# Kernel tuning notes

Measured on AMD Instinct MI355X. Metric: run time of the kernel, lower is better.

The kernel has to match this reference:

```python
import jax, jax.numpy as jnp
import numpy as np
from jax import lax

D_MODEL = 1024
N_GROUPS = 8
SUB_SIZE = 8192
TOP_K = 32
BATCH = 2048


def setup_inputs() -> dict:
    key = jax.random.key(0)
    kx, ke, kb, kd = jax.random.split(key, 4)
    x = jax.random.normal(kx, (BATCH, D_MODEL), dtype=jnp.float32)
    # encoder weights: torch Linear(d_model, size) -> W_enc[g]: [d_model, size]
    W_enc = jax.random.normal(ke, (N_GROUPS, D_MODEL, SUB_SIZE), dtype=jnp.float32) * (1.0 / np.sqrt(D_MODEL))
    b_enc = jax.random.normal(kb, (N_GROUPS, SUB_SIZE), dtype=jnp.float32) * 0.01
    # decoder weights: torch Linear(size, d_model, bias=False).weight is [d_model, size];
    # init normalizes over dim=0 (d_model). We store W_dec[g]: [size, d_model] (= weight.T),
    # so normalize over the last axis.
    W_dec = jax.random.normal(kd, (N_GROUPS, SUB_SIZE, D_MODEL), dtype=jnp.float32)
    W_dec = W_dec / (jnp.linalg.norm(W_dec, axis=-1, keepdims=True) + 1e-8)
    return {"x": x, "W_enc": W_enc, "b_enc": b_enc, "W_dec": W_dec}


def reference(x, W_enc, b_enc, W_dec):
    G, B, S = N_GROUPS, x.shape[0], SUB_SIZE
    # per-group encode: [G, B, S]
    pre = jnp.einsum('bd,gds->gbs', x, W_enc) + b_enc[:, None, :]
    # top-k mask per group (same k for all groups -> batched lax.top_k)
    _, idxs = lax.top_k(pre, TOP_K)  # idxs: [G, B, k]
    gi = jnp.arange(G)[:, None, None]
    bi = jnp.arange(B)[None, :, None]
    mask = jnp.zeros_like(pre).at[gi, bi, idxs].set(1.0)
    acts = jax.nn.relu(pre) * mask  # [G, B, S]
    # per-group decode, summed across groups: [B, d_model]
    final_recon = jnp.einsum('gbs,gsd->bd', acts, W_dec)
    # concatenation of per-group acts along feature dim: [B, G*S]
    full_acts = jnp.transpose(acts, (1, 0, 2)).reshape(B, G * S)
    return (final_recon, full_acts)
```

## Files before the change

kernel.cpp:

```cpp
#include <hip/hip_runtime.h>

#define D_MODEL 1024
#define NGROUPS 8
#define SUB 8192
#define TOPK 32
#define BATCH 2048
#define NTOT (NGROUPS * SUB)

typedef float v4f __attribute__((ext_vector_type(4)));
typedef _Float16 f16x8 __attribute__((ext_vector_type(8)));
typedef _Float16 f16x4 __attribute__((ext_vector_type(4)));
typedef float f32x4 __attribute__((ext_vector_type(4)));

__device__ __forceinline__ unsigned fkey(float f) {
    unsigned u = __float_as_uint(f);
    return (u & 0x80000000u) ? ~u : (u | 0x80000000u);
}
__device__ __forceinline__ float inv_fkey(unsigned key) {
    unsigned u = (key & 0x80000000u) ? (key & 0x7FFFFFFFu) : ~key;
    return __uint_as_float(u);
}

__global__ __launch_bounds__(256) void cvt_x_h(
    const float* __restrict__ x, _Float16* __restrict__ xh)
{
    const size_t i = ((size_t)blockIdx.x * 256 + threadIdx.x) * 8;
    const v4f a = *(const v4f*)(x + i);
    const v4f b = *(const v4f*)(x + i + 4);
    f16x8 h;
#pragma unroll
    for (int j = 0; j < 4; ++j) { h[j] = (_Float16)a[j]; h[4 + j] = (_Float16)b[j]; }
    *(f16x8*)(xh + i) = h;
}

__global__ __launch_bounds__(256) void cvt_wdec_h(
    const float* __restrict__ Wd, _Float16* __restrict__ Wh)
{
    const size_t i = ((size_t)blockIdx.x * 256 + threadIdx.x) * 8;
    const v4f a = *(const v4f*)(Wd + i);
    const v4f b = *(const v4f*)(Wd + i + 4);
    f16x8 h;
#pragma unroll
    for (int j = 0; j < 4; ++j) { h[j] = (_Float16)a[j]; h[4 + j] = (_Float16)b[j]; }
    *(f16x8*)(Wh + i) = h;
}

__global__ __launch_bounds__(256) void transpose_wenc2(
    const float* __restrict__ W, float* __restrict__ WT, _Float16* __restrict__ WhT)
{
    __shared__ float t[32][33];
    const int g = blockIdx.z, kt = blockIdx.y, st = blockIdx.x;
    const int lx = threadIdx.x & 31, ly = threadIdx.x >> 5;
    const float* Wg = W + (size_t)g * D_MODEL * SUB;
    float* WTg = WT + (size_t)g * SUB * D_MODEL;
    _Float16* WhTg = WhT + (size_t)g * SUB * D_MODEL;
#pragma unroll
    for (int r = 0; r < 4; ++r)
        t[ly + 8 * r][lx] = Wg[(size_t)(kt * 32 + ly + 8 * r) * SUB + st * 32 + lx];
    __syncthreads();
#pragma unroll
    for (int r = 0; r < 4; ++r) {
        const float v = t[lx][ly + 8 * r];
        const size_t o = (size_t)(st * 32 + ly + 8 * r) * D_MODEL + kt * 32 + lx;
        WTg[o] = v;
        WhTg[o] = (_Float16)v;
    }
}

__global__ __launch_bounds__(256) void mfma_scores_h2(
    const _Float16* __restrict__ xh, const _Float16* __restrict__ WhT,
    const float* __restrict__ b_enc, float* __restrict__ out_acts)
{
    __shared__ _Float16 Ah[128 * 40];
    __shared__ _Float16 Bh[128 * 40];

    const int tid = threadIdx.x;
    const int wblk = blockIdx.x;
    const int t = (wblk & 7) * 1024 + (wblk >> 3);
    const int mt = t & 15, nt = t >> 4;
    const int g = nt >> 6;
    const int sbase = (nt & 63) * 128;
    const int mbase = mt * 128;

    const int lane = tid & 63, w = tid >> 6;
    const int wm = w >> 1, wn = w & 1;
    const int l15 = lane & 15, grp = lane >> 4;

    const int sr = tid >> 1, kh16 = (tid & 1) * 16;

    const _Float16* Agp = xh + (size_t)mbase * D_MODEL;
    const _Float16* Bgp = WhT + ((size_t)g * SUB + sbase) * D_MODEL;

    f32x4 acc[4][4];
#pragma unroll
    for (int i = 0; i < 4; ++i)
#pragma unroll
        for (int j = 0; j < 4; ++j) acc[i][j] = (f32x4){0.f, 0.f, 0.f, 0.f};

#pragma unroll 1
    for (int it = 0; it < 32; ++it) {
        const int k0 = it * 32;
        const f16x8 a0 = *(const f16x8*)(Agp + (size_t)sr * D_MODEL + k0 + kh16);
        const f16x8 a1 = *(const f16x8*)(Agp + (size_t)sr * D_MODEL + k0 + kh16 + 8);
        const f16x8 b0 = *(const f16x8*)(Bgp + (size_t)sr * D_MODEL + k0 + kh16);
        const f16x8 b1 = *(const f16x8*)(Bgp + (size_t)sr * D_MODEL + k0 + kh16 + 8);

        *(f16x8*)&Ah[sr * 40 + kh16]     = a0;
        *(f16x8*)&Ah[sr * 40 + kh16 + 8] = a1;
        *(f16x8*)&Bh[sr * 40 + kh16]     = b0;
        *(f16x8*)&Bh[sr * 40 + kh16 + 8] = b1;
        __syncthreads();

        f16x8 af[4], bf[4];
#pragma unroll
        for (int i = 0; i < 4; ++i)
            af[i] = *(const f16x8*)&Ah[(wm * 64 + i * 16 + l15) * 40 + 8 * grp];
#pragma unroll
        for (int j = 0; j < 4; ++j)
            bf[j] = *(const f16x8*)&Bh[(wn * 64 + j * 16 + l15) * 40 + 8 * grp];
#pragma unroll
        for (int i = 0; i < 4; ++i)
#pragma unroll
            for (int j = 0; j < 4; ++j)
                acc[i][j] = __builtin_amdgcn_mfma_f32_16x16x32_f16(af[i], bf[j], acc[i][j], 0, 0, 0);
        __syncthreads();
    }

    float bb[4];
#pragma unroll
    for (int j = 0; j < 4; ++j)
        bb[j] = b_enc[(size_t)g * SUB + sbase + wn * 64 + j * 16 + l15];
#pragma unroll
    for (int i = 0; i < 4; ++i) {
        const int row = mbase + wm * 64 + i * 16 + grp * 4;
#pragma unroll
        for (int j = 0; j < 4; ++j) {
            const int cols = sbase + wn * 64 + j * 16 + l15;
#pragma unroll
            for (int r = 0; r < 4; ++r) {
                _Float16* hg = (_Float16*)(out_acts + (size_t)(row + r) * NTOT + (size_t)g * SUB);
                hg[cols] = (_Float16)__fadd_rn(acc[i][j][r], bb[j]);
            }
        }
    }
}

#define CCAP 128
#define BCAP 512

__global__ __launch_bounds__(256) void select_decode_h4(
    const float* __restrict__ x, const float* __restrict__ WT,
    const float* __restrict__ b_enc, const _Float16* __restrict__ Wd_h,
    float* __restrict__ out_recon, float* __restrict__ out_acts)
{
    __shared__ float xrow[1024];
    __shared__ unsigned hist[256], sscan[256], wsum[4];
    __shared__ unsigned sh_bin, sh_above, cert_cnt, band_cnt;
    __shared__ int   cert_idx[CCAP];
    __shared__ float cert_val[CCAP];
    __shared__ int   band_idx[BCAP];
    __shared__ float band_val[BCAP];
    __shared__ int   gcend[4], gbend[4];
    __shared__ int   sel_idx[TOPK];
    __shared__ float sel_val[TOPK];

    const int tid = threadIdx.x;
    const int lane = tid & 63;
    const int w = tid >> 6;
    const size_t b = blockIdx.x >> 1;
    const int h = blockIdx.x & 1;
    const int g0 = h * 4;

    *(float4*)&xrow[tid * 4] = *(const float4*)(x + b * D_MODEL + tid * 4);
    if (tid == 0) { cert_cnt = 0; band_cnt = 0; }
    float r0 = 0.f, r1 = 0.f, r2 = 0.f, r3 = 0.f;

    for (int gi = 0; gi < 4; ++gi) {
        const int g = g0 + gi;
        const _Float16* hg = (const _Float16*)(out_acts + b * NTOT + (size_t)g * SUB);
        float sc[32];
#pragma unroll
        for (int t = 0; t < 4; ++t) {
            const f16x8 hv = *(const f16x8*)(hg + (size_t)(tid + t * 256) * 8);
#pragma unroll
            for (int e = 0; e < 8; ++e) sc[t * 8 + e] = (float)hv[e];
        }

        hist[tid] = 0;
        __syncthreads();
#pragma unroll
        for (int j = 0; j < 32; ++j)
            atomicAdd(&hist[fkey(sc[j]) >> 24], 1u);
        __syncthreads();

        unsigned prefix = 0, kwant = TOPK;
#pragma unroll
        for (int r = 0; r < 2; ++r) {
            unsigned s = hist[tid];
#pragma unroll
            for (int off = 1; off < 64; off <<= 1) {
                const unsigned o = __shfl_down(s, off, 64);
                if (lane + off < 64) s += o;
            }
            if (lane == 0) wsum[w] = s;
            __syncthreads();
            unsigned add = 0;
            for (int w2 = w + 1; w2 < 4; ++w2) add += wsum[w2];
            s += add;
            sscan[tid] = s;
            __syncthreads();
            const unsigned snext = (tid < 255) ? sscan[tid + 1] : 0u;
            if (s >= kwant && snext < kwant) { sh_bin = (unsigned)tid; sh_above = snext; }
            __syncthreads();
            const int shift = 24 - 8 * r;
            prefix |= sh_bin << shift;
            kwant -= sh_above;
            __syncthreads();
            if (r == 0) {
                hist[tid] = 0;
                __syncthreads();
#pragma unroll
                for (int j = 0; j < 32; ++j) {
                    const unsigned key = fkey(sc[j]);
                    if ((key >> 24) == (prefix >> 24))
                        atomicAdd(&hist[(key >> 16) & 255u], 1u);
                }
                __syncthreads();
            }
        }
        const float F = inv_fkey(prefix);
        const unsigned supkey = fkey(F - 0.06f);
        const unsigned inkey  = fkey(F + 0.077f);

#pragma unroll
        for (int j = 0; j < 32; ++j) {
            const unsigned key = fkey(sc[j]);
            if (key >= supkey) {
                const int sidx = (tid + (j >> 3) * 256) * 8 + (j & 7);
                if (key > inkey) {
                    const unsigned slot = atomicAdd(&cert_cnt, 1u);
                    if (slot < CCAP) { cert_idx[slot] = (g << 13) | sidx; cert_val[slot] = fmaxf(sc[j], 0.f); }
                } else {
                    const unsigned slot = atomicAdd(&band_cnt, 1u);
                    if (slot < BCAP) band_idx[slot] = (g << 13) | sidx;
                }
            }
        }
        __syncthreads();
        if (tid == 0) { gcend[gi] = (int)min(cert_cnt, (unsigned)CCAP);
                        gbend[gi] = (int)min(band_cnt, (unsigned)BCAP); }
        __syncthreads();
    }

    float* rowb = out_acts + b * NTOT + (size_t)g0 * SUB;
#pragma unroll 8
    for (int t = 0; t < 32; ++t)
        *(float4*)(rowb + (size_t)(tid + t * 256) * 4) = make_float4(0.f, 0.f, 0.f, 0.f);
    __syncthreads();

    const int bcnt = gbend[3];
    for (int base = 0; base < bcnt; base += 256) {
        const int c = base + tid;
        if (c < bcnt) {
            const int id = band_idx[c];
            const int g = id >> 13, sidx = id & 8191;
            const float* col = WT + ((size_t)g * SUB + sidx) * D_MODEL;
            float a0 = 0.f, a1 = 0.f, a2 = 0.f;
#pragma unroll 4
            for (int q = 0; q < 64; ++q) {
                const float4 w0 = *(const float4*)(col + q * 4);
                const float4 w1 = *(const float4*)(col + 384 + q * 4);
                const float4 w2 = *(const float4*)(col + 768 + q * 4);
                a0 = fmaf(xrow[q * 4 + 0], w0.x, a0); a1 = fmaf(xrow[384 + q * 4 + 0], w1.x, a1); a2 = fmaf(xrow[768 + q * 4 + 0], w2.x, a2);
                a0 = fmaf(xrow[q * 4 + 1], w0.y, a0); a1 = fmaf(xrow[384 + q * 4 + 1], w1.y, a1); a2 = fmaf(xrow[768 + q * 4 + 1], w2.y, a2);
                a0 = fmaf(xrow[q * 4 + 2], w0.z, a0); a1 = fmaf(xrow[384 + q * 4 + 2], w1.z, a1); a2 = fmaf(xrow[768 + q * 4 + 2], w2.z, a2);
                a0 = fmaf(xrow[q * 4 + 3], w0.w, a0); a1 = fmaf(xrow[384 + q * 4 + 3], w1.w, a1); a2 = fmaf(xrow[768 + q * 4 + 3], w2.w, a2);
            }
#pragma unroll 4
            for (int q = 64; q < 96; ++q) {
                const float4 w0 = *(const float4*)(col + q * 4);
                const float4 w1 = *(const float4*)(col + 384 + q * 4);
                a0 = fmaf(xrow[q * 4 + 0], w0.x, a0); a1 = fmaf(xrow[384 + q * 4 + 0], w1.x, a1);
                a0 = fmaf(xrow[q * 4 + 1], w0.y, a0); a1 = fmaf(xrow[384 + q * 4 + 1], w1.y, a1);
                a0 = fmaf(xrow[q * 4 + 2], w0.z, a0); a1 = fmaf(xrow[384 + q * 4 + 2], w1.z, a1);
                a0 = fmaf(xrow[q * 4 + 3], w0.w, a0); a1 = fmaf(xrow[384 + q * 4 + 3], w1.w, a1);
            }
            band_val[c] = __fadd_rn(__fadd_rn(__fadd_rn(a0, a1), a2),
                                    b_enc[(size_t)g * SUB + sidx]);
        }
    }
    __syncthreads();

    for (int gi = 0; gi < 4; ++gi) {
        const int g = g0 + gi;
        const int cb = (gi == 0) ? 0 : gcend[gi - 1];
        const int ce = gcend[gi];
        const int n_in = ce - cb;
        const int n_slots = TOPK - n_in;
        const int bb = (gi == 0) ? 0 : gbend[gi - 1];
        const int be = gbend[gi];

        if (tid < n_in) { sel_idx[tid] = cert_idx[cb + tid] & 8191; sel_val[tid] = cert_val[cb + tid]; }
        for (int t = bb + tid; t < be; t += 256) {
            const unsigned mykey = fkey(band_val[t]);
            const int mys = band_idx[t] & 8191;
            int rank = 0;
            for (int e = bb; e < be; ++e) {
                const unsigned ke = fkey(band_val[e]);
                if (ke > mykey || (ke == mykey && (band_idx[e] & 8191) < mys)) ++rank;
            }
            if (rank < n_slots) { sel_idx[n_in + rank] = mys; sel_val[n_in + rank] = fmaxf(band_val[t], 0.f); }
        }
        __syncthreads();

        float* rowg = out_acts + b * NTOT + (size_t)g * SUB;
        if (tid < TOPK) rowg[sel_idx[tid]] = sel_val[tid];

        const _Float16* Wgh = Wd_h + (size_t)g * SUB * D_MODEL + tid * 4;
#pragma unroll 8
        for (int j = 0; j < TOPK; ++j) {
            const float v = sel_val[j];
            const f16x4 wv = *(const f16x4*)(Wgh + (size_t)sel_idx[j] * D_MODEL);
            r0 = fmaf(v, (float)wv[0], r0); r1 = fmaf(v, (float)wv[1], r1);
            r2 = fmaf(v, (float)wv[2], r2); r3 = fmaf(v, (float)wv[3], r3);
        }
        __syncthreads();
    }
    float* rp = out_recon + b * D_MODEL + tid * 4;
    atomicAdd(rp + 0, r0); atomicAdd(rp + 1, r1);
    atomicAdd(rp + 2, r2); atomicAdd(rp + 3, r3);
}

#define PIDX(s) ((s) + ((s) >> 5))
#define BM 64
#define BN 128
#define BK 16
#define LDSA 68
#define LDSB 132

__global__ __launch_bounds__(256) void fb_encode_gemm(
    const float* __restrict__ x, const float* __restrict__ W_enc,
    const float* __restrict__ b_enc, float* __restrict__ out_acts)
{
    __shared__ float As[BK * LDSA];
    __shared__ float Bs[BK * LDSB];
    const int tid = threadIdx.x;
    const int nt = blockIdx.x, mt = blockIdx.y;
    const int g = nt >> 6, sbase = (nt & 63) * BN, mbase = mt * BM;
    const float* Bp = W_enc + ((size_t)g * D_MODEL) * SUB + sbase;
    const float* Ap = x + (size_t)mbase * D_MODEL;
    const int a_m = tid >> 2, a_c = (tid & 3) * 4;
    const int b_k = tid >> 5, b_c = (tid & 31) * 4;
    const int tr = tid >> 4, tc = tid & 15;
    float tot[4][8], cur[4][8];
#pragma unroll
    for (int i = 0; i < 4; ++i)
#pragma unroll
        for (int j = 0; j < 8; ++j) { tot[i][j] = 0.f; cur[i][j] = 0.f; }
#pragma unroll 1
    for (int it = 0; it < 64; ++it) {
        const int k0 = it * BK;
        const v4f va = *(const v4f*)(Ap + (size_t)a_m * D_MODEL + k0 + a_c);
        const v4f vb0 = *(const v4f*)(Bp + (size_t)(k0 + b_k) * SUB + b_c);
        const v4f vb1 = *(const v4f*)(Bp + (size_t)(k0 + b_k + 8) * SUB + b_c);
#pragma unroll
        for (int j = 0; j < 4; ++j) As[(a_c + j) * LDSA + a_m] = va[j];
        *(v4f*)&Bs[b_k * LDSB + b_c] = vb0;
        *(v4f*)&Bs[(b_k + 8) * LDSB + b_c] = vb1;
        __syncthreads();
        if (it == 24 || it == 48) {
#pragma unroll
            for (int i = 0; i < 4; ++i)
#pragma unroll
                for (int j = 0; j < 8; ++j) { tot[i][j] = __fadd_rn(tot[i][j], cur[i][j]); cur[i][j] = 0.f; }
        }
#pragma unroll
        for (int kk = 0; kk < BK; ++kk) {
            float a[4], bb[8];
            *(v4f*)&a[0] = *(const v4f*)&As[kk * LDSA + tr * 4];
            *(v4f*)&bb[0] = *(const v4f*)&Bs[kk * LDSB + tc * 4];
            *(v4f*)&bb[4] = *(const v4f*)&Bs[kk * LDSB + tc * 4 + 64];
#pragma unroll
            for (int i = 0; i < 4; ++i)
#pragma unroll
                for (int j = 0; j < 8; ++j) cur[i][j] = fmaf(a[i], bb[j], cur[i][j]);
        }
        __syncthreads();
    }
#pragma unroll
    for (int i = 0; i < 4; ++i)
#pragma unroll
        for (int j = 0; j < 8; ++j) tot[i][j] = __fadd_rn(tot[i][j], cur[i][j]);
    const float* bias = b_enc + (size_t)g * SUB + sbase;
    const float4 bb0 = *(const float4*)(bias + tc * 4);
    const float4 bb1 = *(const float4*)(bias + tc * 4 + 64);
    float* outp = out_acts + (size_t)g * SUB + sbase;
#pragma unroll
    for (int i = 0; i < 4; ++i) {
        const size_t row = (size_t)(mbase + tr * 4 + i);
        const float4 o0 = make_float4(__fadd_rn(tot[i][0], bb0.x), __fadd_rn(tot[i][1], bb0.y),
                                      __fadd_rn(tot[i][2], bb0.z), __fadd_rn(tot[i][3], bb0.w));
        const float4 o1 = make_float4(__fadd_rn(tot[i][4], bb1.x), __fadd_rn(tot[i][5], bb1.y),
                                      __fadd_rn(tot[i][6], bb1.z), __fadd_rn(tot[i][7], bb1.w));
        *(float4*)(outp + row * NTOT + tc * 4) = o0;
        *(float4*)(outp + row * NTOT + tc * 4 + 64) = o1;
    }
}

__global__ __launch_bounds__(256) void fb_topk_decode(
    const float* __restrict__ W_dec, float* __restrict__ out_recon,
    float* __restrict__ out_acts)
{
    __shared__ float row[SUB + (SUB >> 5)];
    __shared__ unsigned hist[256], sscan[256], wsum[4], wsum2[4];
    __shared__ unsigned sh_bin, sh_above;
    __shared__ int sel_idx[TOPK];
    __shared__ float sel_val[TOPK];
    const int tid = threadIdx.x, lane = tid & 63, w = tid >> 6;
    const size_t b = blockIdx.x;
    float r0 = 0.f, r1 = 0.f, r2 = 0.f, r3 = 0.f;
    for (int g = 0; g < NGROUPS; ++g) {
        float* rowg = out_acts + b * NTOT + (size_t)g * SUB;
#pragma unroll
        for (int t = 0; t < 8; ++t) {
            const int i4 = tid + t * 256;
            const float4 v = *(const float4*)(rowg + (size_t)i4 * 4);
            const int s0 = i4 * 4;
            row[PIDX(s0) + 0] = v.x; row[PIDX(s0) + 1] = v.y;
            row[PIDX(s0) + 2] = v.z; row[PIDX(s0) + 3] = v.w;
        }
        __syncthreads();
        unsigned prefix = 0, kwant = TOPK;
#pragma unroll
        for (int r = 0; r < 4; ++r) {
            const int shift = 24 - 8 * r;
            hist[tid] = 0;
            __syncthreads();
            for (int j = 0; j < 32; ++j) {
                const unsigned key = fkey(row[tid * 33 + j]);
                const unsigned hi = (unsigned)(((unsigned long long)key) >> (shift + 8));
                const unsigned pi = (unsigned)(((unsigned long long)prefix) >> (shift + 8));
                if (hi == pi) atomicAdd(&hist[(key >> shift) & 255u], 1u);
            }
            __syncthreads();
            unsigned s = hist[tid];
#pragma unroll
            for (int off = 1; off < 64; off <<= 1) {
                const unsigned o = __shfl_down(s, off, 64);
                if (lane + off < 64) s += o;
            }
            if (lane == 0) wsum[w] = s;
            __syncthreads();
            unsigned add = 0;
            for (int w2 = w + 1; w2 < 4; ++w2) add += wsum[w2];
            s += add;
            sscan[tid] = s;
            __syncthreads();
            const unsigned snext = (tid < 255) ? sscan[tid + 1] : 0u;
            if (s >= kwant && snext < kwant) { sh_bin = (unsigned)tid; sh_above = snext; }
            __syncthreads();
            prefix |= sh_bin << shift;
            kwant -= sh_above;
            __syncthreads();
        }
        const unsigned T = prefix, n_take = kwant, cnt_gt_total = TOPK - n_take;
        unsigned loc_gt = 0, loc_eq = 0;
        for (int j = 0; j < 32; ++j) {
            const unsigned key = fkey(row[tid * 33 + j]);
            loc_gt += (key > T); loc_eq += (key == T);
        }
        const unsigned pack = loc_gt | (loc_eq << 16);
        unsigned sI = pack;
#pragma unroll
        for (int off = 1; off < 64; off <<= 1) {
            const unsigned o = __shfl_up(sI, off, 64);
            if (lane >= off) sI += o;
        }
        if (lane == 63) wsum2[w] = sI;
        __syncthreads();
        unsigned woff = 0;
        for (int w2 = 0; w2 < w; ++w2) woff += wsum2[w2];
        const unsigned excl = sI - pack + woff;
        unsigned run_gt = excl & 0xFFFFu, run_eq = excl >> 16;
        for (int j = 0; j < 32; ++j) {
            const int sidx = tid * 32 + j;
            const float f = row[tid * 33 + j];
            const unsigned key = fkey(f);
            const float act = fmaxf(f, 0.f);
            if (key > T) { sel_idx[run_gt] = sidx; sel_val[run_gt] = act; ++run_gt; row[tid * 33 + j] = act; }
            else if (key == T) {
                if (run_eq < n_take) { sel_idx[cnt_gt_total + run_eq] = sidx; sel_val[cnt_gt_total + run_eq] = act; row[tid * 33 + j] = act; }
                else row[tid * 33 + j] = 0.f;
                ++run_eq;
            } else row[tid * 33 + j] = 0.f;
        }
        __syncthreads();
#pragma unroll
        for (int t = 0; t < 8; ++t) {
            const int i4 = tid + t * 256;
            const int s0 = i4 * 4;
            *(float4*)(rowg + (size_t)i4 * 4) =
                make_float4(row[PIDX(s0)], row[PIDX(s0) + 1], row[PIDX(s0) + 2], row[PIDX(s0) + 3]);
        }
        const float* Wg = W_dec + (size_t)g * SUB * D_MODEL + tid * 4;
#pragma unroll 8
        for (int j = 0; j < TOPK; ++j) {
            const float v = sel_val[j];
            const float4 wv = *(const float4*)(Wg + (size_t)sel_idx[j] * D_MODEL);
            r0 = fmaf(v, wv.x, r0); r1 = fmaf(v, wv.y, r1);
            r2 = fmaf(v, wv.z, r2); r3 = fmaf(v, wv.w, r3);
        }
        __syncthreads();
    }
    *(float4*)(out_recon + b * D_MODEL + tid * 4) = make_float4(r0, r1, r2, r3);
}

extern "C" void kernel_launch(void* const* d_in, const int* in_sizes, int n_in,
                              void* d_out, int out_size, void* d_ws, size_t ws_size,
                              hipStream_t stream) {
    const float* x     = (const float*)d_in[0];
    const float* W_enc = (const float*)d_in[1];
    const float* b_enc = (const float*)d_in[2];
    const float* W_dec = (const float*)d_in[3];

    float* out_recon = (float*)d_out;
    float* out_acts  = (float*)d_out + (size_t)BATCH * D_MODEL;

    const size_t WT_BYTES = (size_t)NGROUPS * SUB * D_MODEL * 4;
    const size_t WH_BYTES = (size_t)NGROUPS * SUB * D_MODEL * 2;
    const size_t WD_BYTES = (size_t)NGROUPS * SUB * D_MODEL * 2;
    const size_t XH_BYTES = (size_t)BATCH * D_MODEL * 2;

    if (ws_size >= WT_BYTES + WH_BYTES + WD_BYTES + XH_BYTES) {
        float* WT = (float*)d_ws;
        _Float16* WhT = (_Float16*)((char*)d_ws + WT_BYTES);
        _Float16* WdH = (_Float16*)((char*)d_ws + WT_BYTES + WH_BYTES);
        _Float16* xh  = (_Float16*)((char*)d_ws + WT_BYTES + WH_BYTES + WD_BYTES);
        hipMemsetAsync(out_recon, 0, (size_t)BATCH * D_MODEL * 4, stream);
        cvt_x_h<<<BATCH * D_MODEL / 2048, 256, 0, stream>>>(x, xh);
        cvt_wdec_h<<<NGROUPS * SUB * D_MODEL / 2048, 256, 0, stream>>>(W_dec, WdH);
        transpose_wenc2<<<dim3(SUB / 32, D_MODEL / 32, NGROUPS), 256, 0, stream>>>(W_enc, WT, WhT);
        mfma_scores_h2<<<8192, 256, 0, stream>>>(xh, WhT, b_enc, out_acts);
        select_decode_h4<<<BATCH * 2, 256, 0, stream>>>(x, WT, b_enc, WdH, out_recon, out_acts);
    } else {
        fb_encode_gemm<<<dim3(NTOT / BN, BATCH / BM), 256, 0, stream>>>(x, W_enc, b_enc, out_acts);
        fb_topk_decode<<<BATCH, 256, 0, stream>>>(W_dec, out_recon, out_acts);
    }
}
```

Measured before the change: 1.331 ms.

## Double-buffer LDS in score GEMM and move acts zeroing into it

The fp16 MFMA score kernel now double-buffers its shared-memory tiles, issuing global loads for the next K-slice before computing the current one, so there is one barrier per iteration instead of two. The score kernel also zeroes the unused upper half of each group's fp32 acts region right after writing its fp16 scores. Select_decode therefore only has to zero a smaller slice per group. This shifts zero-fill writes from the select stage into the GEMM epilogue and doubles LDS use per block, which may lower occupancy.

```diff
diff --git a/kernel.cpp b/kernel.cpp
--- a/kernel.cpp
+++ b/kernel.cpp
@@ -67,12 +67,12 @@
     }
 }
 
-__global__ __launch_bounds__(256) void mfma_scores_h2(
+__global__ __launch_bounds__(256) void mfma_scores_h3(
     const _Float16* __restrict__ xh, const _Float16* __restrict__ WhT,
     const float* __restrict__ b_enc, float* __restrict__ out_acts)
 {
-    __shared__ _Float16 Ah[128 * 40];
-    __shared__ _Float16 Bh[128 * 40];
+    __shared__ _Float16 Ah[2][128 * 40];
+    __shared__ _Float16 Bh[2][128 * 40];
 
     const int tid = threadIdx.x;
     const int wblk = blockIdx.x;
@@ -88,41 +88,59 @@
 
     const int sr = tid >> 1, kh16 = (tid & 1) * 16;
 
-    const _Float16* Agp = xh + (size_t)mbase * D_MODEL;
-    const _Float16* Bgp = WhT + ((size_t)g * SUB + sbase) * D_MODEL;
+    const _Float16* Agp = xh + (size_t)mbase * D_MODEL + (size_t)sr * D_MODEL + kh16;
+    const _Float16* Bgp = WhT + ((size_t)g * SUB + sbase) * D_MODEL + (size_t)sr * D_MODEL + kh16;
 
     f32x4 acc[4][4];
 #pragma unroll
     for (int i = 0; i < 4; ++i)
 #pragma unroll
         for (int j = 0; j < 4; ++j) acc[i][j] = (f32x4){0.f, 0.f, 0.f, 0.f};
+
+    {
+        const f16x8 a0 = *(const f16x8*)(Agp);
+        const f16x8 a1 = *(const f16x8*)(Agp + 8);
+        const f16x8 b0 = *(const f16x8*)(Bgp);
+        const f16x8 b1 = *(const f16x8*)(Bgp + 8);
+        *(f16x8*)&Ah[0][sr * 40 + kh16]     = a0;
+        *(f16x8*)&Ah[0][sr * 40 + kh16 + 8] = a1;
+        *(f16x8*)&Bh[0][sr * 40 + kh16]     = b0;
+        *(f16x8*)&Bh[0][sr * 40 + kh16 + 8] = b1;
+        __syncthreads();
+    }
 
 #pragma unroll 1
     for (int it = 0; it < 32; ++it) {
-        const int k0 = it * 32;
-        const f16x8 a0 = *(const f16x8*)(Agp + (size_t)sr * D_MODEL + k0 + kh16);
-        const f16x8 a1 = *(const f16x8*)(Agp + (size_t)sr * D_MODEL + k0 + kh16 + 8);
-        const f16x8 b0 = *(const f16x8*)(Bgp + (size_t)sr * D_MODEL + k0 + kh16);
-        const f16x8 b1 = *(const f16x8*)(Bgp + (size_t)sr * D_MODEL + k0 + kh16 + 8);
-
-        *(f16x8*)&Ah[sr * 40 + kh16]     = a0;
-        *(f16x8*)&Ah[sr * 40 + kh16 + 8] = a1;
-        *(f16x8*)&Bh[sr * 40 + kh16]     = b0;
-        *(f16x8*)&Bh[sr * 40 + kh16 + 8] = b1;
-        __syncthreads();
+        const int cb = it & 1, nb = cb ^ 1;
+        const bool more = (it < 31);
+        f16x8 na0, na1, nb0, nb1;
+        if (more) {
+            const int k0n = (it + 1) * 32;
+            na0 = *(const f16x8*)(Agp + k0n);
+            na1 = *(const f16x8*)(Agp + k0n + 8);
+            nb0 = *(const f16x8*)(Bgp + k0n);
+            nb1 = *(const f16x8*)(Bgp + k0n + 8);
+        }
 
         f16x8 af[4], bf[4];
 #pragma unroll
         for (int i = 0; i < 4; ++i)
-            af[i] = *(const f16x8*)&Ah[(wm * 64 + i * 16 + l15) * 40 + 8 * grp];
+            af[i] = *(const f16x8*)&Ah[cb][(wm * 64 + i * 16 + l15) * 40 + 8 * grp];
 #pragma unroll
         for (int j = 0; j < 4; ++j)
-            bf[j] = *(const f16x8*)&Bh[(wn * 64 + j * 16 + l15) * 40 + 8 * grp];
+            bf[j] = *(const f16x8*)&Bh[cb][(wn * 64 + j * 16 + l15) * 40 + 8 * grp];
 #pragma unroll
         for (int i = 0; i < 4; ++i)
 #pragma unroll
             for (int j = 0; j < 4; ++j)
                 acc[i][j] = __builtin_amdgcn_mfma_f32_16x16x32_f16(af[i], bf[j], acc[i][j], 0, 0, 0);
+
+        if (more) {
+            *(f16x8*)&Ah[nb][sr * 40 + kh16]     = na0;
+            *(f16x8*)&Ah[nb][sr * 40 + kh16 + 8] = na1;
+            *(f16x8*)&Bh[nb][sr * 40 + kh16]     = nb0;
+            *(f16x8*)&Bh[nb][sr * 40 + kh16 + 8] = nb1;
+        }
         __syncthreads();
     }
 
@@ -142,6 +160,17 @@
                 hg[cols] = (_Float16)__fadd_rn(acc[i][j][r], bb[j]);
             }
         }
+    }
+
+    const f16x8 z8 = (f16x8){0, 0, 0, 0, 0, 0, 0, 0};
+#pragma unroll
+    for (int tq = 0; tq < 8; ++tq) {
+        const int vec = tid + tq * 256;
+        const int row = vec >> 4;
+        const int c8 = (vec & 15) * 8;
+        _Float16* p = (_Float16*)(out_acts + (size_t)(mbase + row) * NTOT + (size_t)g * SUB)
+                      + 8192 + sbase + c8;
+        *(f16x8*)p = z8;
     }
 }
 
@@ -252,10 +281,12 @@
         __syncthreads();
     }
 
-    float* rowb = out_acts + b * NTOT + (size_t)g0 * SUB;
-#pragma unroll 8
-    for (int t = 0; t < 32; ++t)
-        *(float4*)(rowb + (size_t)(tid + t * 256) * 4) = make_float4(0.f, 0.f, 0.f, 0.f);
+    for (int gi = 0; gi < 4; ++gi) {
+        float* rz = out_acts + b * NTOT + (size_t)(g0 + gi) * SUB;
+#pragma unroll
+        for (int t = 0; t < 4; ++t)
+            *(float4*)(rz + (size_t)(tid + t * 256) * 4) = make_float4(0.f, 0.f, 0.f, 0.f);
+    }
     __syncthreads();
 
     const int bcnt = gbend[3];
@@ -540,7 +571,7 @@
         cvt_x_h<<<BATCH * D_MODEL / 2048, 256, 0, stream>>>(x, xh);
         cvt_wdec_h<<<NGROUPS * SUB * D_MODEL / 2048, 256, 0, stream>>>(W_dec, WdH);
         transpose_wenc2<<<dim3(SUB / 32, D_MODEL / 32, NGROUPS), 256, 0, stream>>>(W_enc, WT, WhT);
-        mfma_scores_h2<<<8192, 256, 0, stream>>>(xh, WhT, b_enc, out_acts);
+        mfma_scores_h3<<<8192, 256, 0, stream>>>(xh, WhT, b_enc, out_acts);
         select_decode_h4<<<BATCH * 2, 256, 0, stream>>>(x, WT, b_enc, WdH, out_recon, out_acts);
     } else {
         fb_encode_gemm<<<dim3(NTOT / BN, BATCH / BM), 256, 0, stream>>>(x, W_enc, b_enc, out_acts);
```

After: 1.291 ms. 1.03x faster.
